# Performance work log

Measured on AMD Instinct MI355X. Metric: run time of the kernel, lower is better.

The kernel has to match this reference:

```python
import jax, jax.numpy as jnp
import numpy as np
import math

D_MODEL = 256
NHEAD = 8
HEAD = D_MODEL // NHEAD


def make_pe(H, W):
    # temp_bug_fix=False quirk: (-log(1e4)/d_model) // 2 == -1.0 (floor div applied after the divide)
    fac = (-math.log(10000.0) / D_MODEL) // 2
    div = jnp.exp(jnp.arange(0, D_MODEL // 2, 2, dtype=jnp.float32) * fac)[:, None, None]  # [64,1,1]
    xp = jnp.broadcast_to(jnp.arange(1, W + 1, dtype=jnp.float32)[None, :], (H, W))[None]  # [1,H,W]
    yp = jnp.broadcast_to(jnp.arange(1, H + 1, dtype=jnp.float32)[:, None], (H, W))[None]
    pe = jnp.zeros((D_MODEL, H, W), dtype=jnp.float32)
    pe = pe.at[0::4].set(jnp.sin(xp * div))
    pe = pe.at[1::4].set(jnp.cos(xp * div))
    pe = pe.at[2::4].set(jnp.sin(yp * div))
    pe = pe.at[3::4].set(jnp.cos(yp * div))
    return pe[None]  # [1,C,H,W]


def layer_norm(x, g, b, eps=1e-5):
    mu = x.mean(-1, keepdims=True)
    var = ((x - mu) ** 2).mean(-1, keepdims=True)
    return (x - mu) * jax.lax.rsqrt(var + eps) * g + b


def linear_attention(q, k, v, eps=1e-6):
    # q: [N,L,H,D], k/v: [N,S,H,D]
    Q = jax.nn.elu(q) + 1.0
    K = jax.nn.elu(k) + 1.0
    S = v.shape[1]
    v = v / S
    KV = jnp.einsum('nshd,nshv->nhdv', K, v)                      # [N,H,D,D]
    Z = 1.0 / (jnp.einsum('nlhd,nhd->nlh', Q, K.sum(axis=1)) + eps)
    return jnp.einsum('nlhd,nhdv,nlh->nlhv', Q, KV, Z) * S        # [N,L,H,D]


def encoder_layer(x, src, Wq, Wk, Wv, Wm, W1, W2, g1, b1, g2, b2):
    N, L, _ = x.shape
    q = (x @ Wq).reshape(N, L, NHEAD, HEAD)
    k = (src @ Wk).reshape(N, -1, NHEAD, HEAD)
    v = (src @ Wv).reshape(N, -1, NHEAD, HEAD)
    msg = linear_attention(q, k, v).reshape(N, L, D_MODEL) @ Wm
    msg = layer_norm(msg, g1, b1)
    msg = jax.nn.relu(jnp.concatenate([x, msg], axis=-1) @ W1) @ W2
    msg = layer_norm(msg, g2, b2)
    return x + msg


def setup_inputs() -> dict:
    key = jax.random.key(0)
    ks = jax.random.split(key, 10)
    N, H, W = 16, 80, 60
    sc = 1.0 / math.sqrt(D_MODEL)
    return {
        'feat0': jax.random.normal(ks[0], (N, D_MODEL, H, W), dtype=jnp.float32),
        'feat1': jax.random.normal(ks[1], (N, D_MODEL, H, W), dtype=jnp.float32),
        'Wq': jax.random.normal(ks[2], (2, D_MODEL, D_MODEL), dtype=jnp.float32) * sc,
        'Wk': jax.random.normal(ks[3], (2, D_MODEL, D_MODEL), dtype=jnp.float32) * sc,
        'Wv': jax.random.normal(ks[4], (2, D_MODEL, D_MODEL), dtype=jnp.float32) * sc,
        'Wm': jax.random.normal(ks[5], (2, D_MODEL, D_MODEL), dtype=jnp.float32) * sc,
        'W1': jax.random.normal(ks[6], (2, 2 * D_MODEL, D_MODEL), dtype=jnp.float32) * sc,
        'W2': jax.random.normal(ks[7], (2, D_MODEL, D_MODEL), dtype=jnp.float32) * sc,
        'g1': jnp.ones((2, D_MODEL), dtype=jnp.float32),
        'b1': jnp.zeros((2, D_MODEL), dtype=jnp.float32),
        'g2': jnp.ones((2, D_MODEL), dtype=jnp.float32),
        'b2': jnp.zeros((2, D_MODEL), dtype=jnp.float32),
    }


def reference(feat0, feat1, Wq, Wk, Wv, Wm, W1, W2, g1, b1, g2, b2):
    N, C, H, W = feat0.shape
    pe = make_pe(H, W)
    f0 = (feat0 + pe).transpose(0, 2, 3, 1).reshape(N, H * W, C)
    f1 = (feat1 + pe).transpose(0, 2, 3, 1).reshape(N, -1, C)
    for i in range(2):
        f0 = encoder_layer(f0, f1, Wq[i], Wk[i], Wv[i], Wm[i], W1[i], W2[i], g1[i], b1[i], g2[i], b2[i])
    return f0.reshape(N, H, W, C).transpose(0, 3, 1, 2)
```

## Files before the change

kernel.cpp:

```cpp
#include <hip/hip_runtime.h>
#include <math.h>

#define NB 16
#define HH 80
#define WW 60
#define HWSZ (HH * WW)
#define CC 256
#define MTOT (NB * HWSZ)
#define KVF (16 * 8 * 32 * 32)
#define KSF (16 * 8 * 32)
#define BUF ((size_t)MTOT * CC)

typedef unsigned short u16;
typedef __attribute__((ext_vector_type(8))) short short8;
typedef __attribute__((ext_vector_type(4))) float floatx4;

__device__ __forceinline__ float bf2f(u16 u) {
    union { unsigned int i; float f; } v; v.i = ((unsigned int)u) << 16; return v.f;
}
__device__ __forceinline__ u16 f2bf(float f) {
    union { unsigned int i; float f; } v; v.f = f;
    unsigned int u = v.i;
    u += 0x7FFFu + ((u >> 16) & 1u);
    return (u16)(u >> 16);
}
__device__ __forceinline__ float elu1(float x) { return x > 0.f ? x + 1.f : expf(x); }

__device__ __forceinline__ float pe_val(int c, int l) {
    const int h = l / WW, w = l - h * WW;
    const int j = c >> 2, sel = c & 3;
    const float dv = expf(-2.0f * (float)j);
    const float pos = (sel < 2) ? (float)(w + 1) : (float)(h + 1);
    const float arg = pos * dv;
    return (sel & 1) ? cosf(arg) : sinf(arg);
}

__global__ __launch_bounds__(256) void add_pe_transpose(const float* __restrict__ in,
                                                        float* __restrict__ outf,
                                                        u16* __restrict__ outb)
{
    __shared__ float tile[32][33];
    const int n = blockIdx.z;
    const int c0 = blockIdx.y * 32;
    const int l0 = blockIdx.x * 32;
    const int tx = threadIdx.x, ty = threadIdx.y;
#pragma unroll
    for (int i = 0; i < 4; ++i) {
        const int cl = ty + i * 8;
        tile[cl][tx] = in[(size_t)n * CC * HWSZ + (size_t)(c0 + cl) * HWSZ + l0 + tx];
    }
    __syncthreads();
#pragma unroll
    for (int i = 0; i < 4; ++i) {
        const int ll = ty + i * 8;
        const int l = l0 + ll;
        const int c = c0 + tx;
        const float val = tile[tx][ll] + pe_val(c, l);
        const size_t idx = ((size_t)n * HWSZ + l) * CC + c;
        if (outf) outf[idx] = val;
        outb[idx] = f2bf(val);
    }
}

__global__ __launch_bounds__(256) void out_transpose(const float* __restrict__ in,
                                                     float* __restrict__ out)
{
    __shared__ float tile[32][33];
    const int n = blockIdx.z;
    const int c0 = blockIdx.y * 32;
    const int l0 = blockIdx.x * 32;
    const int tx = threadIdx.x, ty = threadIdx.y;
#pragma unroll
    for (int i = 0; i < 4; ++i) {
        const int ll = ty + i * 8;
        tile[ll][tx] = in[((size_t)n * HWSZ + l0 + ll) * CC + c0 + tx];
    }
    __syncthreads();
#pragma unroll
    for (int i = 0; i < 4; ++i) {
        const int cl = ty + i * 8;
        out[(size_t)n * CC * HWSZ + (size_t)(c0 + cl) * HWSZ + l0 + tx] = tile[tx][cl];
    }
}

__global__ __launch_bounds__(256) void convert_wt(const float* __restrict__ W,
                                                  u16* __restrict__ WT, int K)
{
    __shared__ float tile[32][33];
    const int k0 = blockIdx.x * 32;
    const int n0 = blockIdx.y * 32;
    const int tx = threadIdx.x, ty = threadIdx.y;
#pragma unroll
    for (int i = 0; i < 4; ++i)
        tile[ty + i * 8][tx] = W[(size_t)(k0 + ty + i * 8) * 256 + n0 + tx];
    __syncthreads();
#pragma unroll
    for (int i = 0; i < 4; ++i)
        WT[(size_t)(n0 + ty + i * 8) * K + k0 + tx] = f2bf(tile[tx][ty + i * 8]);
}

__global__ __launch_bounds__(256) void zero_kernel(float* __restrict__ p, int n)
{
    const int i = blockIdx.x * 256 + threadIdx.x;
    if (i < n) p[i] = 0.f;
}

__global__ __launch_bounds__(256) void gemm_mfma(const u16* __restrict__ A0,
                                                 const u16* __restrict__ A1,
                                                 const u16* __restrict__ WT,
                                                 u16* __restrict__ C,
                                                 int K, int relu)
{
    __shared__ u16 As[128 * 32];
    __shared__ u16 Bs[128 * 32];
    const int t = threadIdx.x;
    const int row0 = blockIdx.y * 128;
    const int col0 = blockIdx.x * 128;
    const int w = t >> 6, lane = t & 63;
    const int wr = (w >> 1) * 64, wc = (w & 1) * 64;
    const int quad = lane >> 4, lrow = lane & 15;
    const int sm = t >> 2, skc = (t & 3) * 8;

    const floatx4 zero = {0.f, 0.f, 0.f, 0.f};
    floatx4 acc[4][4];
#pragma unroll
    for (int i = 0; i < 4; ++i)
#pragma unroll
        for (int j = 0; j < 4; ++j) acc[i][j] = zero;

    const size_t arow0 = (size_t)(row0 + sm) * 256 + skc;
    const size_t arow1 = (size_t)(row0 + 64 + sm) * 256 + skc;
    const size_t brow0 = (size_t)(col0 + sm) * K + skc;
    const size_t brow1 = (size_t)(col0 + 64 + sm) * K + skc;

    uint4 ra0 = *(const uint4*)(A0 + arow0);
    uint4 ra1 = *(const uint4*)(A0 + arow1);
    uint4 rb0 = *(const uint4*)(WT + brow0);
    uint4 rb1 = *(const uint4*)(WT + brow1);

    for (int k0 = 0; k0 < K; k0 += 32) {
        __syncthreads();
        *(uint4*)&As[sm * 32 + skc] = ra0;
        *(uint4*)&As[(64 + sm) * 32 + skc] = ra1;
        *(uint4*)&Bs[sm * 32 + skc] = rb0;
        *(uint4*)&Bs[(64 + sm) * 32 + skc] = rb1;
        __syncthreads();
        const int kn = k0 + 32;
        if (kn < K) {
            const u16* Abn = (A1 != nullptr && kn >= 256) ? (A1 + (kn - 256)) : (A0 + kn);
            ra0 = *(const uint4*)(Abn + arow0);
            ra1 = *(const uint4*)(Abn + arow1);
            rb0 = *(const uint4*)(WT + brow0 + kn);
            rb1 = *(const uint4*)(WT + brow1 + kn);
        }
        short8 af[4], bfv[4];
#pragma unroll
        for (int i = 0; i < 4; ++i) {
            af[i]  = *(const short8*)&As[(wr + i * 16 + lrow) * 32 + quad * 8];
            bfv[i] = *(const short8*)&Bs[(wc + i * 16 + lrow) * 32 + quad * 8];
        }
#pragma unroll
        for (int i = 0; i < 4; ++i)
#pragma unroll
            for (int j = 0; j < 4; ++j)
                acc[i][j] = __builtin_amdgcn_mfma_f32_16x16x32_bf16(af[i], bfv[j], acc[i][j], 0, 0, 0);
    }

#pragma unroll
    for (int i = 0; i < 4; ++i) {
        const int rbase = row0 + wr + i * 16 + quad * 4;
#pragma unroll
        for (int j = 0; j < 4; ++j) {
            const int cc = col0 + wc + j * 16 + lrow;
#pragma unroll
            for (int r = 0; r < 4; ++r) {
                float x = acc[i][j][r];
                if (relu) x = fmaxf(x, 0.f);
                C[(size_t)(rbase + r) * 256 + cc] = f2bf(x);
            }
        }
    }
}

#define SCHUNK 480
__global__ __launch_bounds__(256) void kv_kernel(const u16* __restrict__ kbuf,
                                                 const u16* __restrict__ vbuf,
                                                 float* __restrict__ KV,
                                                 float* __restrict__ Ksum)
{
    __shared__ float Kls[16][32];
    __shared__ float Vls[16][32];
    const int n = blockIdx.z, h = blockIdx.y;
    const int s0 = blockIdx.x * SCHUNK;
    const int t = threadIdx.x;
    const int lr = t >> 5;
    const int lc = t & 31;
    const int d = t >> 3;
    const int e0 = (t & 7) * 4;
    const float invS = 1.0f / 4800.0f;
    float acc0 = 0.f, acc1 = 0.f, acc2 = 0.f, acc3 = 0.f, ks = 0.f;
    for (int it = 0; it < SCHUNK / 16; ++it) {
        const int sb = s0 + it * 16;
#pragma unroll
        for (int rr = 0; rr < 2; ++rr) {
            const int s = sb + lr + rr * 8;
            const size_t base = ((size_t)(n * HWSZ + s)) * 256 + h * 32 + lc;
            Kls[lr + rr * 8][lc] = elu1(bf2f(kbuf[base]));
            Vls[lr + rr * 8][lc] = bf2f(vbuf[base]) * invS;
        }
        __syncthreads();
#pragma unroll
        for (int ss = 0; ss < 16; ++ss) {
            const float kval = Kls[ss][d];
            acc0 += kval * Vls[ss][e0 + 0];
            acc1 += kval * Vls[ss][e0 + 1];
            acc2 += kval * Vls[ss][e0 + 2];
            acc3 += kval * Vls[ss][e0 + 3];
            if (e0 == 0) ks += kval;
        }
        __syncthreads();
    }
    float* kvp = KV + ((size_t)(n * 8 + h) * 32 + d) * 32 + e0;
    atomicAdd(kvp + 0, acc0);
    atomicAdd(kvp + 1, acc1);
    atomicAdd(kvp + 2, acc2);
    atomicAdd(kvp + 3, acc3);
    if (e0 == 0) atomicAdd(&Ksum[(size_t)(n * 8 + h) * 32 + d], ks);
}

#define AR 32
__global__ __launch_bounds__(256) void attn_apply(u16* __restrict__ q,
                                                  const float* __restrict__ KV,
                                                  const float* __restrict__ Ksum)
{
    const int row0 = blockIdx.x * AR;
    const int n = row0 / HWSZ;
    const int t = threadIdx.x;
    const int h = t >> 5, e = t & 31;
    __shared__ float Qls[AR][256];
    __shared__ float Ks[256];

    float kvr[32];
    const float* kvp = KV + (size_t)(n * 8 + h) * 1024 + e;
#pragma unroll
    for (int d = 0; d < 32; ++d) kvr[d] = kvp[d * 32];
    Ks[t] = Ksum[(size_t)n * 256 + t];

    const int lrow = t >> 5;
    const int lcol = (t & 31) * 8;
#pragma unroll
    for (int rr = 0; rr < 4; ++rr) {
        const int r = rr * 8 + lrow;
        const ushort4 u0 = *(const ushort4*)&q[(size_t)(row0 + r) * 256 + lcol];
        const ushort4 u1 = *(const ushort4*)&q[(size_t)(row0 + r) * 256 + lcol + 4];
        Qls[r][lcol + 0] = elu1(bf2f(u0.x));
        Qls[r][lcol + 1] = elu1(bf2f(u0.y));
        Qls[r][lcol + 2] = elu1(bf2f(u0.z));
        Qls[r][lcol + 3] = elu1(bf2f(u0.w));
        Qls[r][lcol + 4] = elu1(bf2f(u1.x));
        Qls[r][lcol + 5] = elu1(bf2f(u1.y));
        Qls[r][lcol + 6] = elu1(bf2f(u1.z));
        Qls[r][lcol + 7] = elu1(bf2f(u1.w));
    }
    __syncthreads();

    for (int r = 0; r < AR; ++r) {
        float zden = 1e-6f, acc = 0.f;
#pragma unroll
        for (int d = 0; d < 32; ++d) {
            const float qd = Qls[r][h * 32 + d];
            zden += qd * Ks[h * 32 + d];
            acc += qd * kvr[d];
        }
        q[(size_t)(row0 + r) * 256 + t] = f2bf(acc * (4800.0f / zden));
    }
}

__device__ __forceinline__ float wave_sum(float v)
{
#pragma unroll
    for (int off = 32; off > 0; off >>= 1) v += __shfl_xor(v, off, 64);
    return v;
}

__global__ __launch_bounds__(256) void ln_inplace(u16* __restrict__ x,
                                                  const float* __restrict__ g,
                                                  const float* __restrict__ b)
{
    const int t = threadIdx.x;
    const int wv = t >> 6, lane = t & 63;
    const int row0 = blockIdx.x * 32 + wv * 8;
    const int c0 = lane * 4;
    const float4 gv = *(const float4*)&g[c0];
    const float4 bv = *(const float4*)&b[c0];
#pragma unroll
    for (int r = 0; r < 8; ++r) {
        const size_t base = (size_t)(row0 + r) * 256 + c0;
        const ushort4 u = *(const ushort4*)&x[base];
        const float v0 = bf2f(u.x), v1 = bf2f(u.y), v2 = bf2f(u.z), v3 = bf2f(u.w);
        const float mu = wave_sum(v0 + v1 + v2 + v3) * (1.0f / 256.0f);
        const float d0 = v0 - mu, d1 = v1 - mu, d2 = v2 - mu, d3 = v3 - mu;
        const float var = wave_sum(d0 * d0 + d1 * d1 + d2 * d2 + d3 * d3) * (1.0f / 256.0f);
        const float rst = rsqrtf(var + 1e-5f);
        ushort4 o;
        o.x = f2bf(d0 * rst * gv.x + bv.x);
        o.y = f2bf(d1 * rst * gv.y + bv.y);
        o.z = f2bf(d2 * rst * gv.z + bv.z);
        o.w = f2bf(d3 * rst * gv.w + bv.w);
        *(ushort4*)&x[base] = o;
    }
}

__global__ __launch_bounds__(256) void ln_resid(const u16* __restrict__ x,
                                                const float* __restrict__ g,
                                                const float* __restrict__ b,
                                                float* __restrict__ f0,
                                                u16* __restrict__ f0b)
{
    const int t = threadIdx.x;
    const int wv = t >> 6, lane = t & 63;
    const int row0 = blockIdx.x * 32 + wv * 8;
    const int c0 = lane * 4;
    const float4 gv = *(const float4*)&g[c0];
    const float4 bv = *(const float4*)&b[c0];
#pragma unroll
    for (int r = 0; r < 8; ++r) {
        const size_t base = (size_t)(row0 + r) * 256 + c0;
        const ushort4 u = *(const ushort4*)&x[base];
        const float v0 = bf2f(u.x), v1 = bf2f(u.y), v2 = bf2f(u.z), v3 = bf2f(u.w);
        const float mu = wave_sum(v0 + v1 + v2 + v3) * (1.0f / 256.0f);
        const float d0 = v0 - mu, d1 = v1 - mu, d2 = v2 - mu, d3 = v3 - mu;
        const float var = wave_sum(d0 * d0 + d1 * d1 + d2 * d2 + d3 * d3) * (1.0f / 256.0f);
        const float rst = rsqrtf(var + 1e-5f);
        float4 f = *(const float4*)&f0[base];
        f.x += d0 * rst * gv.x + bv.x;
        f.y += d1 * rst * gv.y + bv.y;
        f.z += d2 * rst * gv.z + bv.z;
        f.w += d3 * rst * gv.w + bv.w;
        *(float4*)&f0[base] = f;
        ushort4 o;
        o.x = f2bf(f.x); o.y = f2bf(f.y); o.z = f2bf(f.z); o.w = f2bf(f.w);
        *(ushort4*)&f0b[base] = o;
    }
}

extern "C" void kernel_launch(void* const* d_in, const int* in_sizes, int n_in,
                              void* d_out, int out_size, void* d_ws, size_t ws_size,
                              hipStream_t stream)
{
    const float* feat0 = (const float*)d_in[0];
    const float* feat1 = (const float*)d_in[1];
    const float* Wq = (const float*)d_in[2];
    const float* Wk = (const float*)d_in[3];
    const float* Wv = (const float*)d_in[4];
    const float* Wm = (const float*)d_in[5];
    const float* W1 = (const float*)d_in[6];
    const float* W2 = (const float*)d_in[7];
    const float* g1 = (const float*)d_in[8];
    const float* b1 = (const float*)d_in[9];
    const float* g2 = (const float*)d_in[10];
    const float* b2 = (const float*)d_in[11];

    float* ws = (float*)d_ws;
    float* KV = ws;
    float* Ksum = KV + KVF;
    u16* Wb = (u16*)(Ksum + KSF);
    const size_t WBE = 458752;
    float* f0 = ws + (KVF + KSF) + WBE;
    u16* f0b = (u16*)(f0 + BUF);
    u16* f1b = f0b + BUF;
    u16* kb16 = (u16*)d_out;
    u16* vb16 = kb16 + BUF;

    const dim3 tb(32, 8);
    const dim3 tgrid(HWSZ / 32, CC / 32, NB);
    add_pe_transpose<<<tgrid, tb, 0, stream>>>(feat0, f0, f0b);
    add_pe_transpose<<<tgrid, tb, 0, stream>>>(feat1, nullptr, f1b);

    for (int i = 0; i < 2; ++i) {
        u16* WqT = Wb + (size_t)i * WBE;
        u16* WkT = WqT + 65536;
        u16* WvT = WkT + 65536;
        u16* WmT = WvT + 65536;
        u16* W1T = WmT + 65536;
        u16* W2T = W1T + 131072;
        convert_wt<<<dim3(8, 8),  tb, 0, stream>>>(Wq + (size_t)i * 65536,  WqT, 256);
        convert_wt<<<dim3(8, 8),  tb, 0, stream>>>(Wk + (size_t)i * 65536,  WkT, 256);
        convert_wt<<<dim3(8, 8),  tb, 0, stream>>>(Wv + (size_t)i * 65536,  WvT, 256);
        convert_wt<<<dim3(8, 8),  tb, 0, stream>>>(Wm + (size_t)i * 65536,  WmT, 256);
        convert_wt<<<dim3(16, 8), tb, 0, stream>>>(W1 + (size_t)i * 131072, W1T, 512);
        convert_wt<<<dim3(8, 8),  tb, 0, stream>>>(W2 + (size_t)i * 65536,  W2T, 256);
    }

    const dim3 ggrid(2, MTOT / 128);
    for (int i = 0; i < 2; ++i) {
        u16* WqT = Wb + (size_t)i * WBE;
        u16* WkT = WqT + 65536;
        u16* WvT = WkT + 65536;
        u16* WmT = WvT + 65536;
        u16* W1T = WmT + 65536;
        u16* W2T = W1T + 131072;

        gemm_mfma<<<ggrid, 256, 0, stream>>>(f1b, nullptr, WkT, kb16, 256, 0);
        gemm_mfma<<<ggrid, 256, 0, stream>>>(f1b, nullptr, WvT, vb16, 256, 0);

        zero_kernel<<<(KVF + KSF + 255) / 256, 256, 0, stream>>>(KV, KVF + KSF);
        kv_kernel<<<dim3(HWSZ / SCHUNK, 8, NB), 256, 0, stream>>>(kb16, vb16, KV, Ksum);

        gemm_mfma<<<ggrid, 256, 0, stream>>>(f0b, nullptr, WqT, kb16, 256, 0);
        attn_apply<<<MTOT / AR, 256, 0, stream>>>(kb16, KV, Ksum);

        gemm_mfma<<<ggrid, 256, 0, stream>>>(kb16, nullptr, WmT, vb16, 256, 0);
        ln_inplace<<<MTOT / 32, 256, 0, stream>>>(vb16, g1 + i * 256, b1 + i * 256);

        gemm_mfma<<<ggrid, 256, 0, stream>>>(f0b, vb16, W1T, kb16, 512, 1);
        gemm_mfma<<<ggrid, 256, 0, stream>>>(kb16, nullptr, W2T, vb16, 256, 0);
        ln_resid<<<MTOT / 32, 256, 0, stream>>>(vb16, g2 + i * 256, b2 + i * 256, f0, f0b);
    }

    out_transpose<<<tgrid, tb, 0, stream>>>(f0, (float*)d_out);
}
```

Baseline: 901.3 us.

## Compute attention apply with MFMA using split-bf16 KV matrices

Adds a kv_finalize kernel that transposes the per-head KV matrix and splits it into high and low bf16 parts. attn_apply now runs Q·KV as MFMA 16x16x32 bf16 instructions, with Q kept in registers, instead of scalar FMA loops over a shared-memory Q tile. The normalizer is computed per lane and reduced with shuffles. The aim is to move the attention-apply FLOPs onto matrix cores. In exchange it adds one small kernel launch, and rounding Q to bf16 costs some precision.

After: 844.3 us. 1.07x faster.

```diff
diff --git a/kernel.cpp b/kernel.cpp
--- a/kernel.cpp
+++ b/kernel.cpp
@@ -228,51 +228,82 @@
     if (e0 == 0) atomicAdd(&Ksum[(size_t)(n * 8 + h) * 32 + d], ks);
 }
 
-#define AR 32
+__global__ __launch_bounds__(256) void kv_finalize(const float* __restrict__ KV,
+                                                   u16* __restrict__ KVThi,
+                                                   u16* __restrict__ KVTlo)
+{
+    const int nh = blockIdx.x;
+    const int t = threadIdx.x;
+    const int d = t >> 3, e0 = (t & 7) * 4;
+    const float4 v = *(const float4*)&KV[(size_t)nh * 1024 + d * 32 + e0];
+    const float vv[4] = {v.x, v.y, v.z, v.w};
+#pragma unroll
+    for (int j = 0; j < 4; ++j) {
+        const int e = e0 + j;
+        const float x = vv[j];
+        const u16 hi = f2bf(x);
+        const float lo = x - bf2f(hi);
+        KVThi[(size_t)nh * 1024 + e * 32 + d] = hi;
+        KVTlo[(size_t)nh * 1024 + e * 32 + d] = f2bf(lo);
+    }
+}
+
 __global__ __launch_bounds__(256) void attn_apply(u16* __restrict__ q,
-                                                  const float* __restrict__ KV,
+                                                  const u16* __restrict__ KVThi,
+                                                  const u16* __restrict__ KVTlo,
                                                   const float* __restrict__ Ksum)
 {
-    const int row0 = blockIdx.x * AR;
-    const int n = row0 / HWSZ;
-    const int t = threadIdx.x;
-    const int h = t >> 5, e = t & 31;
-    __shared__ float Qls[AR][256];
+    const int t = threadIdx.x;
+    const int row0b = blockIdx.x * 64;
+    const int n = row0b / HWSZ;
+    const int w = t >> 6, lane = t & 63;
+    const int quad = lane >> 4, lrow = lane & 15;
+    const int row0 = row0b + w * 16;
+
     __shared__ float Ks[256];
-
-    float kvr[32];
-    const float* kvp = KV + (size_t)(n * 8 + h) * 1024 + e;
-#pragma unroll
-    for (int d = 0; d < 32; ++d) kvr[d] = kvp[d * 32];
     Ks[t] = Ksum[(size_t)n * 256 + t];
-
-    const int lrow = t >> 5;
-    const int lcol = (t & 31) * 8;
-#pragma unroll
-    for (int rr = 0; rr < 4; ++rr) {
-        const int r = rr * 8 + lrow;
-        const ushort4 u0 = *(const ushort4*)&q[(size_t)(row0 + r) * 256 + lcol];
-        const ushort4 u1 = *(const ushort4*)&q[(size_t)(row0 + r) * 256 + lcol + 4];
-        Qls[r][lcol + 0] = elu1(bf2f(u0.x));
-        Qls[r][lcol + 1] = elu1(bf2f(u0.y));
-        Qls[r][lcol + 2] = elu1(bf2f(u0.z));
-        Qls[r][lcol + 3] = elu1(bf2f(u0.w));
-        Qls[r][lcol + 4] = elu1(bf2f(u1.x));
-        Qls[r][lcol + 5] = elu1(bf2f(u1.y));
-        Qls[r][lcol + 6] = elu1(bf2f(u1.z));
-        Qls[r][lcol + 7] = elu1(bf2f(u1.w));
-    }
     __syncthreads();
 
-    for (int r = 0; r < AR; ++r) {
-        float zden = 1e-6f, acc = 0.f;
-#pragma unroll
-        for (int d = 0; d < 32; ++d) {
-            const float qd = Qls[r][h * 32 + d];
-            zden += qd * Ks[h * 32 + d];
-            acc += qd * kvr[d];
-        }
-        q[(size_t)(row0 + r) * 256 + t] = f2bf(acc * (4800.0f / zden));
+    const floatx4 zero = {0.f, 0.f, 0.f, 0.f};
+#pragma unroll
+    for (int h = 0; h < 8; ++h) {
+        const size_t qoff = (size_t)(row0 + lrow) * 256 + h * 32 + quad * 8;
+        const ushort4 u0 = *(const ushort4*)&q[qoff];
+        const ushort4 u1 = *(const ushort4*)&q[qoff + 4];
+        float qf[8];
+        qf[0] = elu1(bf2f(u0.x)); qf[1] = elu1(bf2f(u0.y));
+        qf[2] = elu1(bf2f(u0.z)); qf[3] = elu1(bf2f(u0.w));
+        qf[4] = elu1(bf2f(u1.x)); qf[5] = elu1(bf2f(u1.y));
+        qf[6] = elu1(bf2f(u1.z)); qf[7] = elu1(bf2f(u1.w));
+        short8 a;
+#pragma unroll
+        for (int j = 0; j < 8; ++j) a[j] = (short)f2bf(qf[j]);
+
+        float zp = 0.f;
+#pragma unroll
+        for (int j = 0; j < 8; ++j) zp += qf[j] * Ks[h * 32 + quad * 8 + j];
+        zp += __shfl_xor(zp, 16, 64);
+        zp += __shfl_xor(zp, 32, 64);
+
+        const size_t kvb = (size_t)(n * 8 + h) * 32;
+        const short8 bh0 = *(const short8*)&KVThi[(kvb + lrow) * 32 + quad * 8];
+        const short8 bh1 = *(const short8*)&KVThi[(kvb + 16 + lrow) * 32 + quad * 8];
+        const short8 bl0 = *(const short8*)&KVTlo[(kvb + lrow) * 32 + quad * 8];
+        const short8 bl1 = *(const short8*)&KVTlo[(kvb + 16 + lrow) * 32 + quad * 8];
+
+        floatx4 acc0 = __builtin_amdgcn_mfma_f32_16x16x32_bf16(a, bh0, zero, 0, 0, 0);
+        acc0 = __builtin_amdgcn_mfma_f32_16x16x32_bf16(a, bl0, acc0, 0, 0, 0);
+        floatx4 acc1 = __builtin_amdgcn_mfma_f32_16x16x32_bf16(a, bh1, zero, 0, 0, 0);
+        acc1 = __builtin_amdgcn_mfma_f32_16x16x32_bf16(a, bl1, acc1, 0, 0, 0);
+
+#pragma unroll
+        for (int r = 0; r < 4; ++r) {
+            const float zden = __shfl(zp, quad * 4 + r, 64);
+            const float sc = 4800.0f / (zden + 1e-6f);
+            const size_t ob = (size_t)(row0 + quad * 4 + r) * 256 + h * 32;
+            q[ob + lrow]      = f2bf(acc0[r] * sc);
+            q[ob + 16 + lrow] = f2bf(acc1[r] * sc);
+        }
     }
 }
 
@@ -369,6 +400,8 @@
     float* f0 = ws + (KVF + KSF) + WBE;
     u16* f0b = (u16*)(f0 + BUF);
     u16* f1b = f0b + BUF;
+    u16* KVThi = f1b + BUF;
+    u16* KVTlo = KVThi + KVF;
     u16* kb16 = (u16*)d_out;
     u16* vb16 = kb16 + BUF;
 
@@ -406,9 +439,10 @@
 
         zero_kernel<<<(KVF + KSF + 255) / 256, 256, 0, stream>>>(KV, KVF + KSF);
         kv_kernel<<<dim3(HWSZ / SCHUNK, 8, NB), 256, 0, stream>>>(kb16, vb16, KV, Ksum);
+        kv_finalize<<<128, 256, 0, stream>>>(KV, KVThi, KVTlo);
 
         gemm_mfma<<<ggrid, 256, 0, stream>>>(f0b, nullptr, WqT, kb16, 256, 0);
-        attn_apply<<<MTOT / AR, 256, 0, stream>>>(kb16, KV, Ksum);
+        attn_apply<<<MTOT / 64, 256, 0, stream>>>(kb16, KVThi, KVTlo, Ksum);
 
         gemm_mfma<<<ggrid, 256, 0, stream>>>(kb16, nullptr, WmT, vb16, 256, 0);
         ln_inplace<<<MTOT / 32, 256, 0, stream>>>(vb16, g1 + i * 256, b1 + i * 256);
```
